# Kernel optimization log

Hardware: AMD Instinct MI355X
Metric: run time of the kernel (lower is better)

## Reference

```python
import jax, jax.numpy as jnp
import numpy as np

D_MODEL = 1024
N_HEADS = 16
D_HEAD = D_MODEL // N_HEADS
BLOCK = 128
B, T = 2, 2048


def setup_inputs() -> dict:
    key = jax.random.key(0)
    ks = jax.random.split(key, 5)
    x = jax.random.normal(ks[0], (B, T, D_MODEL), dtype=jnp.float32)
    def init_w(k):
        # nn.Linear default init scale ~ 1/sqrt(fan_in)
        return jax.random.normal(k, (D_MODEL, D_MODEL), dtype=jnp.float32) / np.sqrt(D_MODEL).astype(np.float32)
    return {
        "x": x,
        "Wq": init_w(ks[1]),
        "Wk": init_w(ks[2]),
        "Wv": init_w(ks[3]),
        "Wo": init_w(ks[4]),
    }


def _flash_attention(Q, K, V, block_size, scale):
    """Online-softmax tiled attention over kv blocks (causal). Q,K,V: (B,H,T,d)."""
    Bb, H, Tt, d = Q.shape
    n_blocks = Tt // block_size
    # (n_blocks, B, H, block, d) so scan streams kv tiles
    Kb = K.reshape(Bb, H, n_blocks, block_size, d).transpose(2, 0, 1, 3, 4)
    Vb = V.reshape(Bb, H, n_blocks, block_size, d).transpose(2, 0, 1, 3, 4)
    starts = jnp.arange(n_blocks) * block_size
    q_pos = jnp.arange(Tt)

    def step(carry, xs):
        m, l, acc = carry
        kb, vb, st = xs
        # scores: (B,H,T,block)
        scores = scale * jnp.einsum('bhtd,bhsd->bhts', Q, kb)
        kv_pos = st + jnp.arange(block_size)
        future = kv_pos[None, :] > q_pos[:, None]          # (T, block)
        scores = jnp.where(future[None, None], -jnp.inf, scores)
        m_new = jnp.maximum(m, jnp.max(scores, axis=-1, keepdims=True))
        p = jnp.exp(scores - m_new)
        corr = jnp.exp(m - m_new)
        l = corr * l + jnp.sum(p, axis=-1, keepdims=True)
        acc = corr * acc + jnp.einsum('bhts,bhsd->bhtd', p, vb)
        return (m_new, l, acc), None

    m0 = jnp.full((Bb, H, Tt, 1), -jnp.inf, dtype=jnp.float32)
    l0 = jnp.zeros((Bb, H, Tt, 1), dtype=jnp.float32)
    a0 = jnp.zeros((Bb, H, Tt, d), dtype=jnp.float32)
    (m, l, acc), _ = jax.lax.scan(step, (m0, l0, a0), (Kb, Vb, starts))
    return acc / jnp.maximum(l, 1e-12)


def reference(x, Wq, Wk, Wv, Wo):
    Bx, Tx, _ = x.shape
    scale = 1.0 / np.sqrt(D_HEAD).astype(np.float32)
    def proj(W):  # nn.Linear: y = x @ W.T
        y = jnp.einsum('btm,nm->btn', x, W)
        return y.reshape(Bx, Tx, N_HEADS, D_HEAD).transpose(0, 2, 1, 3)
    Q, K, V = proj(Wq), proj(Wk), proj(Wv)
    O = _flash_attention(Q.astype(jnp.float32), K.astype(jnp.float32), V.astype(jnp.float32), BLOCK, scale)
    O = O.astype(x.dtype).transpose(0, 2, 1, 3).reshape(Bx, Tx, D_MODEL)
    return jnp.einsum('btm,nm->btn', O, Wo)
```

## Files before the change

kernel.cpp:

```cpp
#include <hip/hip_runtime.h>
#include <hip/hip_bf16.h>

typedef __attribute__((ext_vector_type(8))) short short8;
typedef __attribute__((ext_vector_type(4))) float f32x4;
typedef __attribute__((ext_vector_type(4))) unsigned int uint4v;
typedef unsigned short u16;

#define MFMA_BF16(a, b, c) __builtin_amdgcn_mfma_f32_16x16x32_bf16(a, b, c, 0, 0, 0)

#define T_SEQ 2048
#define DMODEL 1024
#define NHEADS 16
#define DHEAD 64
#define NEG_BIG (-30000.0f)

__device__ __forceinline__ unsigned bfr(unsigned u) {
  return (u + 0x7fffu + ((u >> 16) & 1u)) >> 16;
}
__device__ __forceinline__ uint4v ld8bf(const float* __restrict__ p) {
  const uint4v a = *(const uint4v*)p;
  const uint4v b = *(const uint4v*)(p + 4);
  uint4v r;
  r[0] = bfr(a[0]) | (bfr(a[1]) << 16);
  r[1] = bfr(a[2]) | (bfr(a[3]) << 16);
  r[2] = bfr(b[0]) | (bfr(b[1]) << 16);
  r[3] = bfr(b[2]) | (bfr(b[3]) << 16);
  return r;
}
__device__ __forceinline__ u16 f2bf(float f) {
  unsigned u = __float_as_uint(f);
  u += 0x7fffu + ((u >> 16) & 1u);
  return (u16)(u >> 16);
}

__device__ __forceinline__ float dpp16_max(float x) {
  float t;
  t = __int_as_float(__builtin_amdgcn_update_dpp(0, __float_as_int(x), 0xB1, 0xF, 0xF, true));
  x = fmaxf(x, t);
  t = __int_as_float(__builtin_amdgcn_update_dpp(0, __float_as_int(x), 0x4E, 0xF, 0xF, true));
  x = fmaxf(x, t);
  t = __int_as_float(__builtin_amdgcn_update_dpp(0, __float_as_int(x), 0x124, 0xF, 0xF, true));
  x = fmaxf(x, t);
  t = __int_as_float(__builtin_amdgcn_update_dpp(0, __float_as_int(x), 0x128, 0xF, 0xF, true));
  x = fmaxf(x, t);
  return x;
}
__device__ __forceinline__ float dpp16_sum(float x) {
  float t;
  t = __int_as_float(__builtin_amdgcn_update_dpp(0, __float_as_int(x), 0xB1, 0xF, 0xF, true));
  x += t;
  t = __int_as_float(__builtin_amdgcn_update_dpp(0, __float_as_int(x), 0x4E, 0xF, 0xF, true));
  x += t;
  t = __int_as_float(__builtin_amdgcn_update_dpp(0, __float_as_int(x), 0x124, 0xF, 0xF, true));
  x += t;
  t = __int_as_float(__builtin_amdgcn_update_dpp(0, __float_as_int(x), 0x128, 0xF, 0xF, true));
  x += t;
  return x;
}

__global__ __launch_bounds__(256) void cvt_all(
    const float* __restrict__ x, const float* __restrict__ wq,
    const float* __restrict__ wk, const float* __restrict__ wv,
    const float* __restrict__ wo, u16* __restrict__ xh, u16* __restrict__ wqh,
    u16* __restrict__ wkh, u16* __restrict__ wvh, u16* __restrict__ woh) {
  int bi = blockIdx.x;
  const float* s;
  u16* d;
  size_t base;
  if (bi < 2048) {
    s = x; d = xh; base = (size_t)bi * 2048;
  } else {
    int k = (bi - 2048) >> 9;
    int r = (bi - 2048) & 511;
    s = (k == 0) ? wq : (k == 1) ? wk : (k == 2) ? wv : wo;
    d = (k == 0) ? wqh : (k == 1) ? wkh : (k == 2) ? wvh : woh;
    base = (size_t)r * 2048;
  }
  size_t i = base + (size_t)threadIdx.x * 8;
  *(uint4v*)&d[i] = ld8bf(&s[i]);
}

__global__ __launch_bounds__(256) void gemm_qkv(
    const u16* __restrict__ X, const u16* __restrict__ Wq,
    const u16* __restrict__ Wk, const u16* __restrict__ Wv,
    u16* __restrict__ Qo, u16* __restrict__ Ko, u16* __restrict__ Vo) {
  __shared__ u16 As[128 * 32];
  __shared__ u16 Bs[128 * 32];
  const int tid = threadIdx.x, lane = tid & 63, w = tid >> 6;
  const int wm = (w >> 1) * 64, wn = (w & 1) * 64;
  const int lrow = lane & 15;
  const int lk = (lane >> 4) << 3;
  const int lq = (lane >> 4) << 2;
  const int mBase = blockIdx.x * 128, nBase = blockIdx.y * 128;
  const u16* Bt = (blockIdx.z == 0) ? Wq : (blockIdx.z == 1) ? Wk : Wv;
  u16* D = (blockIdx.z == 0) ? Qo : (blockIdx.z == 1) ? Ko : Vo;
  const float scale = (blockIdx.z == 0) ? 0.125f : 1.0f;

  f32x4 acc[4][4];
#pragma unroll
  for (int mi = 0; mi < 4; mi++)
#pragma unroll
    for (int ni = 0; ni < 4; ni++) acc[mi][ni] = (f32x4)0.0f;

  for (int k0 = 0; k0 < 1024; k0 += 32) {
    __syncthreads();
#pragma unroll
    for (int i = 0; i < 2; i++) {
      int c = i * 256 + tid;
      int r = c >> 2, kk = (c & 3) << 3;
      *(uint4v*)&As[c * 8] = *(const uint4v*)&X[(size_t)(mBase + r) * 1024 + k0 + kk];
      *(uint4v*)&Bs[c * 8] = *(const uint4v*)&Bt[(size_t)(nBase + r) * 1024 + k0 + kk];
    }
    __syncthreads();
    short8 af[4], bf[4];
#pragma unroll
    for (int mi = 0; mi < 4; mi++)
      af[mi] = *(const short8*)&As[(wm + mi * 16 + lrow) * 32 + lk];
#pragma unroll
    for (int ni = 0; ni < 4; ni++)
      bf[ni] = *(const short8*)&Bs[(wn + ni * 16 + lrow) * 32 + lk];
#pragma unroll
    for (int mi = 0; mi < 4; mi++)
#pragma unroll
      for (int ni = 0; ni < 4; ni++)
        acc[mi][ni] = MFMA_BF16(af[mi], bf[ni], acc[mi][ni]);
  }
#pragma unroll
  for (int mi = 0; mi < 4; mi++)
#pragma unroll
    for (int r = 0; r < 4; r++) {
      int m = mBase + wm + mi * 16 + lq + r;
      int b = m >> 11, t = m & 2047;
#pragma unroll
      for (int ni = 0; ni < 4; ni++) {
        int n = nBase + wn + ni * 16 + lrow;
        int h = n >> 6, dd = n & 63;
        D[(((size_t)(b * NHEADS + h)) * T_SEQ + t) * DHEAD + dd] =
            f2bf(acc[mi][ni][r] * scale);
      }
    }
}

__global__ __launch_bounds__(256) void attn_snake(
    const u16* __restrict__ Qg, const u16* __restrict__ Kg,
    const u16* __restrict__ Vg, u16* __restrict__ Ob) {
  __shared__ u16 smem[13824];
  u16* Qs = smem;
  u16* Ps = smem;
  u16* Ks = smem + 4608;
  u16* Vt = smem + 9216;

  const int tid = threadIdx.x;
  const int w = tid >> 6, lane = tid & 63;
  const int lrow = lane & 15;
  const int lk = (lane >> 4) << 3;
  const int lq = (lane >> 4) << 2;

  const int j = blockIdx.x;
  const int bh = blockIdx.y;
  const int b = bh >> 4, h = bh & 15;
  const u16* Qp = Qg + (size_t)bh * T_SEQ * DHEAD;
  const u16* Kp = Kg + (size_t)bh * T_SEQ * DHEAD;
  const u16* Vp = Vg + (size_t)bh * T_SEQ * DHEAD;

#pragma unroll
  for (int p = 0; p < 2; p++) {
    const int qt = p ? (31 - j) : j;
    const int qb = qt * 64;

    __syncthreads();
#pragma unroll
    for (int i = 0; i < 2; i++) {
      int c = i * 256 + tid;
      int r = c >> 3, kk = (c & 7) << 3;
      *(uint4v*)&Qs[r * 72 + kk] =
          *(const uint4v*)&Qp[(size_t)(qb + r) * DHEAD + kk];
    }
    __syncthreads();
    short8 qf[2];
#pragma unroll
    for (int ks = 0; ks < 2; ks++)
      qf[ks] = *(const short8*)&Qs[(w * 16 + lrow) * 72 + ks * 32 + lk];

    float mst[4], lst[4];
    f32x4 oacc[4];
#pragma unroll
    for (int r = 0; r < 4; r++) { mst[r] = NEG_BIG; lst[r] = 0.f; }
#pragma unroll
    for (int nd = 0; nd < 4; nd++) oacc[nd] = (f32x4)0.0f;

    const int ntiles = qt + 1;
    for (int kt = 0; kt < ntiles; kt++) {
      const int kvb = kt * 64;
      __syncthreads();
#pragma unroll
      for (int i = 0; i < 2; i++) {
        int c = i * 256 + tid;
        int r = c >> 3, kk = (c & 7) << 3;
        *(uint4v*)&Ks[r * 72 + kk] =
            *(const uint4v*)&Kp[(size_t)(kvb + r) * DHEAD + kk];
      }
#pragma unroll
      for (int i = 0; i < 2; i++) {
        int t2 = i * 256 + tid;
        int d = t2 & 63, c8 = t2 >> 6;
        int kv0 = c8 << 3;
        short8 v8;
#pragma unroll
        for (int jj = 0; jj < 8; jj++)
          v8[jj] = (short)Vp[(size_t)(kvb + kv0 + jj) * DHEAD + d];
        *(short8*)&Vt[d * 72 + kv0] = v8;
      }
      __syncthreads();

      f32x4 s[4];
#pragma unroll
      for (int nt = 0; nt < 4; nt++) {
        f32x4 a = (f32x4)0.0f;
#pragma unroll
        for (int ks = 0; ks < 2; ks++) {
          short8 kf = *(const short8*)&Ks[(nt * 16 + lrow) * 72 + ks * 32 + lk];
          a = MFMA_BF16(qf[ks], kf, a);
        }
        s[nt] = a;
      }

      const int rowb = qb + w * 16 + lq;
      float corr[4], lt[4];
#pragma unroll
      for (int r = 0; r < 4; r++) {
        float mx = NEG_BIG;
#pragma unroll
        for (int nt = 0; nt < 4; nt++) {
          int col = kvb + nt * 16 + lrow;
          float sv = s[nt][r];
          if (col > rowb + r) sv = NEG_BIG;
          s[nt][r] = sv;
          mx = fmaxf(mx, sv);
        }
        mx = dpp16_max(mx);
        float mn = fmaxf(mst[r], mx);
        corr[r] = __expf(mst[r] - mn);
        mst[r] = mn;
        float ls = 0.f;
#pragma unroll
        for (int nt = 0; nt < 4; nt++) {
          float pp = __expf(s[nt][r] - mn);
          s[nt][r] = pp;
          ls += pp;
        }
        lt[r] = dpp16_sum(ls);
      }
#pragma unroll
      for (int r = 0; r < 4; r++) {
        lst[r] = corr[r] * lst[r] + lt[r];
#pragma unroll
        for (int nd = 0; nd < 4; nd++) oacc[nd][r] *= corr[r];
#pragma unroll
        for (int nt = 0; nt < 4; nt++)
          Ps[(w * 16 + lq + r) * 72 + nt * 16 + lrow] = f2bf(s[nt][r]);
      }

#pragma unroll
      for (int ks = 0; ks < 2; ks++) {
        short8 vf[4];
#pragma unroll
        for (int nd = 0; nd < 4; nd++)
          vf[nd] = *(const short8*)&Vt[(nd * 16 + lrow) * 72 + ks * 32 + lk];
        short8 pf = *(const short8*)&Ps[(w * 16 + lrow) * 72 + ks * 32 + lk];
#pragma unroll
        for (int nd = 0; nd < 4; nd++)
          oacc[nd] = MFMA_BF16(pf, vf[nd], oacc[nd]);
      }
    }

#pragma unroll
    for (int r = 0; r < 4; r++) {
      int t = qb + w * 16 + lq + r;
      float inv = 1.f / lst[r];
#pragma unroll
      for (int nd = 0; nd < 4; nd++)
        Ob[((size_t)(b * T_SEQ + t)) * DMODEL + h * DHEAD + nd * 16 + lrow] =
            f2bf(oacc[nd][r] * inv);
    }
  }
}

__global__ __launch_bounds__(256) void gemm_out_bf(const u16* __restrict__ O,
                                                   const u16* __restrict__ Wo,
                                                   float* __restrict__ Out) {
  __shared__ u16 As[128 * 32];
  __shared__ u16 Bs[128 * 32];
  const int tid = threadIdx.x, lane = tid & 63, w = tid >> 6;
  const int wm = (w >> 1) * 64, wn = (w & 1) * 64;
  const int lrow = lane & 15;
  const int lk = (lane >> 4) << 3;
  const int lq = (lane >> 4) << 2;
  const int mBase = blockIdx.x * 128, nBase = blockIdx.y * 128;

  f32x4 acc[4][4];
#pragma unroll
  for (int mi = 0; mi < 4; mi++)
#pragma unroll
    for (int ni = 0; ni < 4; ni++) acc[mi][ni] = (f32x4)0.0f;

  for (int k0 = 0; k0 < 1024; k0 += 32) {
    __syncthreads();
#pragma unroll
    for (int i = 0; i < 2; i++) {
      int c = i * 256 + tid;
      int r = c >> 2, kk = (c & 3) << 3;
      *(uint4v*)&As[c * 8] = *(const uint4v*)&O[(size_t)(mBase + r) * 1024 + k0 + kk];
      *(uint4v*)&Bs[c * 8] = *(const uint4v*)&Wo[(size_t)(nBase + r) * 1024 + k0 + kk];
    }
    __syncthreads();
    short8 af[4], bf[4];
#pragma unroll
    for (int mi = 0; mi < 4; mi++)
      af[mi] = *(const short8*)&As[(wm + mi * 16 + lrow) * 32 + lk];
#pragma unroll
    for (int ni = 0; ni < 4; ni++)
      bf[ni] = *(const short8*)&Bs[(wn + ni * 16 + lrow) * 32 + lk];
#pragma unroll
    for (int mi = 0; mi < 4; mi++)
#pragma unroll
      for (int ni = 0; ni < 4; ni++)
        acc[mi][ni] = MFMA_BF16(af[mi], bf[ni], acc[mi][ni]);
  }
#pragma unroll
  for (int mi = 0; mi < 4; mi++)
#pragma unroll
    for (int r = 0; r < 4; r++) {
      int m = mBase + wm + mi * 16 + lq + r;
#pragma unroll
      for (int ni = 0; ni < 4; ni++)
        Out[(size_t)m * DMODEL + nBase + wn + ni * 16 + lrow] = acc[mi][ni][r];
    }
}

extern "C" void kernel_launch(void* const* d_in, const int* in_sizes, int n_in,
                              void* d_out, int out_size, void* d_ws,
                              size_t ws_size, hipStream_t stream) {
  const float* x = (const float*)d_in[0];
  const float* Wq = (const float*)d_in[1];
  const float* Wk = (const float*)d_in[2];
  const float* Wv = (const float*)d_in[3];
  const float* Wo = (const float*)d_in[4];
  float* out = (float*)d_out;

  u16* xh = (u16*)d_ws;
  u16* wqh = xh + 4194304;
  u16* wkh = wqh + 1048576;
  u16* wvh = wkh + 1048576;
  u16* woh = wvh + 1048576;
  u16* Q = woh + 1048576;
  u16* K = Q + 4194304;
  u16* V = K + 4194304;
  u16* O = V + 4194304;

  cvt_all<<<dim3(4096), 256, 0, stream>>>(x, Wq, Wk, Wv, Wo, xh, wqh, wkh, wvh, woh);
  gemm_qkv<<<dim3(32, 8, 3), 256, 0, stream>>>(xh, wqh, wkh, wvh, Q, K, V);
  attn_snake<<<dim3(16, 32), 256, 0, stream>>>(Q, K, V, O);
  gemm_out_bf<<<dim3(32, 8), 256, 0, stream>>>(O, woh, out);
}
```

Measured before the change: 208.7 us.

## Transpose V in QKV GEMM, swap attention MFMA operands, use direct-to-LDS loads

After: 196.3 us. 5.9% less time.

```diff
diff --git a/kernel.cpp b/kernel.cpp
--- a/kernel.cpp
+++ b/kernel.cpp
@@ -3,6 +3,7 @@
 
 typedef __attribute__((ext_vector_type(8))) short short8;
 typedef __attribute__((ext_vector_type(4))) float f32x4;
+typedef __attribute__((ext_vector_type(2))) unsigned int uint2v;
 typedef __attribute__((ext_vector_type(4))) unsigned int uint4v;
 typedef unsigned short u16;
 
@@ -13,6 +14,13 @@
 #define NHEADS 16
 #define DHEAD 64
 #define NEG_BIG (-30000.0f)
+#define QSCALE 0.1803368801111f
+
+#if __has_builtin(__builtin_amdgcn_exp2f)
+#define EXP2(x) __builtin_amdgcn_exp2f(x)
+#else
+#define EXP2(x) exp2f(x)
+#endif
 
 __device__ __forceinline__ unsigned bfr(unsigned u) {
   return (u + 0x7fffu + ((u >> 16) & 1u)) >> 16;
@@ -32,30 +40,10 @@
   u += 0x7fffu + ((u >> 16) & 1u);
   return (u16)(u >> 16);
 }
-
-__device__ __forceinline__ float dpp16_max(float x) {
-  float t;
-  t = __int_as_float(__builtin_amdgcn_update_dpp(0, __float_as_int(x), 0xB1, 0xF, 0xF, true));
-  x = fmaxf(x, t);
-  t = __int_as_float(__builtin_amdgcn_update_dpp(0, __float_as_int(x), 0x4E, 0xF, 0xF, true));
-  x = fmaxf(x, t);
-  t = __int_as_float(__builtin_amdgcn_update_dpp(0, __float_as_int(x), 0x124, 0xF, 0xF, true));
-  x = fmaxf(x, t);
-  t = __int_as_float(__builtin_amdgcn_update_dpp(0, __float_as_int(x), 0x128, 0xF, 0xF, true));
-  x = fmaxf(x, t);
-  return x;
-}
-__device__ __forceinline__ float dpp16_sum(float x) {
-  float t;
-  t = __int_as_float(__builtin_amdgcn_update_dpp(0, __float_as_int(x), 0xB1, 0xF, 0xF, true));
-  x += t;
-  t = __int_as_float(__builtin_amdgcn_update_dpp(0, __float_as_int(x), 0x4E, 0xF, 0xF, true));
-  x += t;
-  t = __int_as_float(__builtin_amdgcn_update_dpp(0, __float_as_int(x), 0x124, 0xF, 0xF, true));
-  x += t;
-  t = __int_as_float(__builtin_amdgcn_update_dpp(0, __float_as_int(x), 0x128, 0xF, 0xF, true));
-  x += t;
-  return x;
+__device__ __forceinline__ void gld16(const u16* g, u16* l) {
+  __builtin_amdgcn_global_load_lds(
+      (const __attribute__((address_space(1))) unsigned int*)g,
+      (__attribute__((address_space(3))) unsigned int*)l, 16, 0, 0);
 }
 
 __global__ __launch_bounds__(256) void cvt_all(
@@ -84,8 +72,8 @@
     const u16* __restrict__ X, const u16* __restrict__ Wq,
     const u16* __restrict__ Wk, const u16* __restrict__ Wv,
     u16* __restrict__ Qo, u16* __restrict__ Ko, u16* __restrict__ Vo) {
-  __shared__ u16 As[128 * 32];
-  __shared__ u16 Bs[128 * 32];
+  __shared__ __attribute__((aligned(16))) u16 As[128 * 32];
+  __shared__ __attribute__((aligned(16))) u16 Bs[128 * 32];
   const int tid = threadIdx.x, lane = tid & 63, w = tid >> 6;
   const int wm = (w >> 1) * 64, wn = (w & 1) * 64;
   const int lrow = lane & 15;
@@ -94,7 +82,7 @@
   const int mBase = blockIdx.x * 128, nBase = blockIdx.y * 128;
   const u16* Bt = (blockIdx.z == 0) ? Wq : (blockIdx.z == 1) ? Wk : Wv;
   u16* D = (blockIdx.z == 0) ? Qo : (blockIdx.z == 1) ? Ko : Vo;
-  const float scale = (blockIdx.z == 0) ? 0.125f : 1.0f;
+  const float scale = (blockIdx.z == 0) ? QSCALE : 1.0f;
 
   f32x4 acc[4][4];
 #pragma unroll
@@ -108,8 +96,8 @@
     for (int i = 0; i < 2; i++) {
       int c = i * 256 + tid;
       int r = c >> 2, kk = (c & 3) << 3;
-      *(uint4v*)&As[c * 8] = *(const uint4v*)&X[(size_t)(mBase + r) * 1024 + k0 + kk];
-      *(uint4v*)&Bs[c * 8] = *(const uint4v*)&Bt[(size_t)(nBase + r) * 1024 + k0 + kk];
+      gld16(&X[(size_t)(mBase + r) * 1024 + k0 + kk], &As[c * 8]);
+      gld16(&Bt[(size_t)(nBase + r) * 1024 + k0 + kk], &Bs[c * 8]);
     }
     __syncthreads();
     short8 af[4], bf[4];
@@ -125,6 +113,7 @@
       for (int ni = 0; ni < 4; ni++)
         acc[mi][ni] = MFMA_BF16(af[mi], bf[ni], acc[mi][ni]);
   }
+  const int vz = (blockIdx.z == 2);
 #pragma unroll
   for (int mi = 0; mi < 4; mi++)
 #pragma unroll
@@ -135,16 +124,17 @@
       for (int ni = 0; ni < 4; ni++) {
         int n = nBase + wn + ni * 16 + lrow;
         int h = n >> 6, dd = n & 63;
-        D[(((size_t)(b * NHEADS + h)) * T_SEQ + t) * DHEAD + dd] =
-            f2bf(acc[mi][ni][r] * scale);
+        size_t idx = vz ? (((size_t)((b * NHEADS + h) * DHEAD + dd)) * T_SEQ + t)
+                        : ((((size_t)(b * NHEADS + h)) * T_SEQ + t) * DHEAD + dd);
+        D[idx] = f2bf(acc[mi][ni][r] * scale);
       }
     }
 }
 
 __global__ __launch_bounds__(256) void attn_snake(
     const u16* __restrict__ Qg, const u16* __restrict__ Kg,
-    const u16* __restrict__ Vg, u16* __restrict__ Ob) {
-  __shared__ u16 smem[13824];
+    const u16* __restrict__ Vtg, u16* __restrict__ Ob) {
+  __shared__ __attribute__((aligned(16))) u16 smem[13824];
   u16* Qs = smem;
   u16* Ps = smem;
   u16* Ks = smem + 4608;
@@ -153,15 +143,16 @@
   const int tid = threadIdx.x;
   const int w = tid >> 6, lane = tid & 63;
   const int lrow = lane & 15;
-  const int lk = (lane >> 4) << 3;
-  const int lq = (lane >> 4) << 2;
+  const int quad = lane >> 4;
+  const int lk = quad << 3;
+  const int q_local = w * 16 + lrow;
 
   const int j = blockIdx.x;
   const int bh = blockIdx.y;
   const int b = bh >> 4, h = bh & 15;
   const u16* Qp = Qg + (size_t)bh * T_SEQ * DHEAD;
   const u16* Kp = Kg + (size_t)bh * T_SEQ * DHEAD;
-  const u16* Vp = Vg + (size_t)bh * T_SEQ * DHEAD;
+  const u16* Vp = Vtg + (size_t)bh * DHEAD * T_SEQ;
 
 #pragma unroll
   for (int p = 0; p < 2; p++) {
@@ -180,12 +171,10 @@
     short8 qf[2];
 #pragma unroll
     for (int ks = 0; ks < 2; ks++)
-      qf[ks] = *(const short8*)&Qs[(w * 16 + lrow) * 72 + ks * 32 + lk];
-
-    float mst[4], lst[4];
+      qf[ks] = *(const short8*)&Qs[q_local * 72 + ks * 32 + lk];
+
+    float mst = NEG_BIG, lst = 0.f;
     f32x4 oacc[4];
-#pragma unroll
-    for (int r = 0; r < 4; r++) { mst[r] = NEG_BIG; lst[r] = 0.f; }
 #pragma unroll
     for (int nd = 0; nd < 4; nd++) oacc[nd] = (f32x4)0.0f;
 
@@ -199,89 +188,87 @@
         int r = c >> 3, kk = (c & 7) << 3;
         *(uint4v*)&Ks[r * 72 + kk] =
             *(const uint4v*)&Kp[(size_t)(kvb + r) * DHEAD + kk];
-      }
-#pragma unroll
-      for (int i = 0; i < 2; i++) {
-        int t2 = i * 256 + tid;
-        int d = t2 & 63, c8 = t2 >> 6;
-        int kv0 = c8 << 3;
-        short8 v8;
-#pragma unroll
-        for (int jj = 0; jj < 8; jj++)
-          v8[jj] = (short)Vp[(size_t)(kvb + kv0 + jj) * DHEAD + d];
-        *(short8*)&Vt[d * 72 + kv0] = v8;
+        *(uint4v*)&Vt[r * 72 + kk] =
+            *(const uint4v*)&Vp[(size_t)r * T_SEQ + kvb + kk];
       }
       __syncthreads();
 
       f32x4 s[4];
 #pragma unroll
-      for (int nt = 0; nt < 4; nt++) {
+      for (int kvt = 0; kvt < 4; kvt++) {
         f32x4 a = (f32x4)0.0f;
 #pragma unroll
         for (int ks = 0; ks < 2; ks++) {
-          short8 kf = *(const short8*)&Ks[(nt * 16 + lrow) * 72 + ks * 32 + lk];
-          a = MFMA_BF16(qf[ks], kf, a);
+          short8 kf = *(const short8*)&Ks[(kvt * 16 + lrow) * 72 + ks * 32 + lk];
+          a = MFMA_BF16(kf, qf[ks], a);
         }
-        s[nt] = a;
-      }
-
-      const int rowb = qb + w * 16 + lq;
-      float corr[4], lt[4];
-#pragma unroll
-      for (int r = 0; r < 4; r++) {
-        float mx = NEG_BIG;
-#pragma unroll
-        for (int nt = 0; nt < 4; nt++) {
-          int col = kvb + nt * 16 + lrow;
-          float sv = s[nt][r];
-          if (col > rowb + r) sv = NEG_BIG;
-          s[nt][r] = sv;
-          mx = fmaxf(mx, sv);
+        s[kvt] = a;
+      }
+
+      if (kt == qt) {
+#pragma unroll
+        for (int kvt = 0; kvt < 4; kvt++)
+#pragma unroll
+          for (int r = 0; r < 4; r++)
+            if (kvt * 16 + quad * 4 + r > q_local) s[kvt][r] = NEG_BIG;
+      }
+
+      float mx = s[0][0];
+#pragma unroll
+      for (int kvt = 0; kvt < 4; kvt++)
+#pragma unroll
+        for (int r = 0; r < 4; r++) mx = fmaxf(mx, s[kvt][r]);
+      mx = fmaxf(mx, __shfl_xor(mx, 16));
+      mx = fmaxf(mx, __shfl_xor(mx, 32));
+      float mn = fmaxf(mst, mx);
+      float corr = EXP2(mst - mn);
+      mst = mn;
+      float ls = 0.f;
+#pragma unroll
+      for (int kvt = 0; kvt < 4; kvt++)
+#pragma unroll
+        for (int r = 0; r < 4; r++) {
+          float pv = EXP2(s[kvt][r] - mn);
+          s[kvt][r] = pv;
+          ls += pv;
         }
-        mx = dpp16_max(mx);
-        float mn = fmaxf(mst[r], mx);
-        corr[r] = __expf(mst[r] - mn);
-        mst[r] = mn;
-        float ls = 0.f;
-#pragma unroll
-        for (int nt = 0; nt < 4; nt++) {
-          float pp = __expf(s[nt][r] - mn);
-          s[nt][r] = pp;
-          ls += pp;
+      ls += __shfl_xor(ls, 16);
+      ls += __shfl_xor(ls, 32);
+      lst = corr * lst + ls;
+#pragma unroll
+      for (int nd = 0; nd < 4; nd++) oacc[nd] *= corr;
+
+#pragma unroll
+      for (int kvt = 0; kvt < 4; kvt++) {
+        uint2v pk;
+        pk[0] = (__float_as_uint(s[kvt][0]) >> 16) |
+                (__float_as_uint(s[kvt][1]) & 0xffff0000u);
+        pk[1] = (__float_as_uint(s[kvt][2]) >> 16) |
+                (__float_as_uint(s[kvt][3]) & 0xffff0000u);
+        *(uint2v*)&Ps[q_local * 72 + kvt * 16 + quad * 4] = pk;
+      }
+
+#pragma unroll
+      for (int ks = 0; ks < 2; ks++) {
+        short8 pf = *(const short8*)&Ps[q_local * 72 + ks * 32 + lk];
+#pragma unroll
+        for (int nd = 0; nd < 4; nd++) {
+          short8 vf = *(const short8*)&Vt[(nd * 16 + lrow) * 72 + ks * 32 + lk];
+          oacc[nd] = MFMA_BF16(vf, pf, oacc[nd]);
         }
-        lt[r] = dpp16_sum(ls);
-      }
-#pragma unroll
-      for (int r = 0; r < 4; r++) {
-        lst[r] = corr[r] * lst[r] + lt[r];
-#pragma unroll
-        for (int nd = 0; nd < 4; nd++) oacc[nd][r] *= corr[r];
-#pragma unroll
-        for (int nt = 0; nt < 4; nt++)
-          Ps[(w * 16 + lq + r) * 72 + nt * 16 + lrow] = f2bf(s[nt][r]);
-      }
-
-#pragma unroll
-      for (int ks = 0; ks < 2; ks++) {
-        short8 vf[4];
-#pragma unroll
-        for (int nd = 0; nd < 4; nd++)
-          vf[nd] = *(const short8*)&Vt[(nd * 16 + lrow) * 72 + ks * 32 + lk];
-        short8 pf = *(const short8*)&Ps[(w * 16 + lrow) * 72 + ks * 32 + lk];
-#pragma unroll
-        for (int nd = 0; nd < 4; nd++)
-          oacc[nd] = MFMA_BF16(pf, vf[nd], oacc[nd]);
-      }
-    }
-
-#pragma unroll
-    for (int r = 0; r < 4; r++) {
-      int t = qb + w * 16 + lq + r;
-      float inv = 1.f / lst[r];
-#pragma unroll
-      for (int nd = 0; nd < 4; nd++)
-        Ob[((size_t)(b * T_SEQ + t)) * DMODEL + h * DHEAD + nd * 16 + lrow] =
-            f2bf(oacc[nd][r] * inv);
+      }
+    }
+
+    float inv = 1.f / lst;
+    size_t rowbase = ((size_t)(b * T_SEQ + qb + q_local)) * DMODEL + h * DHEAD;
+#pragma unroll
+    for (int nd = 0; nd < 4; nd++) {
+      uint2v pk;
+      pk[0] = (unsigned)f2bf(oacc[nd][0] * inv) |
+              ((unsigned)f2bf(oacc[nd][1] * inv) << 16);
+      pk[1] = (unsigned)f2bf(oacc[nd][2] * inv) |
+              ((unsigned)f2bf(oacc[nd][3] * inv) << 16);
+      *(uint2v*)&Ob[rowbase + nd * 16 + quad * 4] = pk;
     }
   }
 }
@@ -289,8 +276,8 @@
 __global__ __launch_bounds__(256) void gemm_out_bf(const u16* __restrict__ O,
                                                    const u16* __restrict__ Wo,
                                                    float* __restrict__ Out) {
-  __shared__ u16 As[128 * 32];
-  __shared__ u16 Bs[128 * 32];
+  __shared__ __attribute__((aligned(16))) u16 As[128 * 32];
+  __shared__ __attribute__((aligned(16))) u16 Bs[128 * 32];
   const int tid = threadIdx.x, lane = tid & 63, w = tid >> 6;
   const int wm = (w >> 1) * 64, wn = (w & 1) * 64;
   const int lrow = lane & 15;
@@ -310,8 +297,8 @@
     for (int i = 0; i < 2; i++) {
       int c = i * 256 + tid;
       int r = c >> 2, kk = (c & 3) << 3;
-      *(uint4v*)&As[c * 8] = *(const uint4v*)&O[(size_t)(mBase + r) * 1024 + k0 + kk];
-      *(uint4v*)&Bs[c * 8] = *(const uint4v*)&Wo[(size_t)(nBase + r) * 1024 + k0 + kk];
+      gld16(&O[(size_t)(mBase + r) * 1024 + k0 + kk], &As[c * 8]);
+      gld16(&Wo[(size_t)(nBase + r) * 1024 + k0 + kk], &Bs[c * 8]);
     }
     __syncthreads();
     short8 af[4], bf[4];
```
